# Kernel tuning notes

Measured on AMD Instinct MI355X. Metric: run time of the kernel, lower is better.

Reference implementation:

```python
import jax, jax.numpy as jnp
import numpy as np

B, T, F, H, L = 16384, 24, 7, 8, 4
DENSE = [T * H, 1024, 2048, 4]


def setup_inputs() -> dict:
    key = jax.random.key(0)
    d = {"x": jax.random.normal(jax.random.fold_in(key, 0), (B, T, F), jnp.float32)}
    k = 1
    s = 1.0 / np.sqrt(H)  # torch LSTM init bound
    for l in range(L):
        in_dim = F if l == 0 else H
        for name, shape in [("Wih", (4 * H, in_dim)), ("Whh", (4 * H, H)), ("bih", (4 * H,)), ("bhh", (4 * H,))]:
            d[f"{name}{l}"] = jax.random.uniform(jax.random.fold_in(key, k), shape, jnp.float32, -s, s)
            k += 1
    for i in range(1, len(DENSE)):
        si = 1.0 / np.sqrt(DENSE[i - 1])
        d[f"Wd{i}"] = jax.random.uniform(jax.random.fold_in(key, k), (DENSE[i], DENSE[i - 1]), jnp.float32, -si, si)
        k += 1
        d[f"bd{i}"] = jax.random.uniform(jax.random.fold_in(key, k), (DENSE[i],), jnp.float32, -si, si)
        k += 1
    return d


def _lstm_layer(xs, Wih, Whh, b):
    # xs: [T, B, in] -> ys: [T, B, H]; torch gate order i,f,g,o
    Hn = Whh.shape[1]
    h0 = jnp.zeros((xs.shape[1], Hn), xs.dtype)

    def step(carry, xt):
        h, c = carry
        z = xt @ Wih.T + h @ Whh.T + b  # [B, 4H]
        i, f, g, o = jnp.split(z, 4, axis=-1)
        c = jax.nn.sigmoid(f) * c + jax.nn.sigmoid(i) * jnp.tanh(g)
        h = jax.nn.sigmoid(o) * jnp.tanh(c)
        return (h, c), h

    (_, _), ys = jax.lax.scan(step, (h0, h0), xs)
    return ys


def _forward(x, lstm_params, dense_params):
    xs = jnp.transpose(x, (1, 0, 2))  # [T, B, F]
    for (Wih, Whh, bih, bhh) in lstm_params:
        xs = _lstm_layer(xs, Wih, Whh, bih + bhh)
    out = jnp.transpose(xs, (1, 0, 2)).reshape(x.shape[0], T * H)  # [B, 192]
    (W1, b1), (W2, b2), (W3, b3) = dense_params
    out = jax.nn.relu(out @ W1.T + b1)
    out = jax.nn.relu(out @ W2.T + b2)
    return out @ W3.T + b3  # [B, num_classes]


def reference(x, Wih0, Whh0, bih0, bhh0, Wih1, Whh1, bih1, bhh1, Wih2, Whh2, bih2, bhh2, Wih3, Whh3, bih3, bhh3, Wd1, bd1, Wd2, bd2, Wd3, bd3):
    lstm_params = [(Wih0, Whh0, bih0, bhh0), (Wih1, Whh1, bih1, bhh1), (Wih2, Whh2, bih2, bhh2), (Wih3, Whh3, bih3, bhh3)]
    dense_params = [(Wd1, bd1), (Wd2, bd2), (Wd3, bd3)]
    return _forward(x, lstm_params, dense_params)
```

## Files before the change

kernel.cpp:

```cpp
#include <hip/hip_runtime.h>
#include <hip/hip_bf16.h>

typedef __attribute__((ext_vector_type(4))) float f32x4;
typedef __attribute__((ext_vector_type(2))) float f32x2;
typedef __attribute__((ext_vector_type(8))) short bf16x8;

__device__ __forceinline__ ushort f2bf(float f) {
    union { float f; uint u; } v; v.f = f;
    uint u = v.u;
    return (ushort)((u + 0x7fffu + ((u >> 16) & 1u)) >> 16);
}
__device__ __forceinline__ float sigm(float x) {
    return __builtin_amdgcn_rcpf(1.0f + __builtin_amdgcn_exp2f(x * -1.442695040888963f));
}
__device__ __forceinline__ float tanh_(float x) {
    return 2.0f * __builtin_amdgcn_rcpf(1.0f + __builtin_amdgcn_exp2f(x * -2.885390081777927f)) - 1.0f;
}

typedef const __attribute__((address_space(1))) unsigned int ga_u32;
typedef __attribute__((address_space(3))) unsigned int lds_u32;
__device__ __forceinline__ void g2l16(const void* g, void* l) {
    __builtin_amdgcn_global_load_lds((ga_u32*)(unsigned long long)g,
                                     (lds_u32*)(unsigned int)(unsigned long long)l,
                                     16, 0, 0);
}

struct LstmW {
    const float* wih[4];
    const float* whh[4];
    const float* bih[4];
    const float* bhh[4];
};

__device__ __forceinline__ void gates8p(const f32x2 w01[8], const f32x2 w23[8],
                                        const float xv8[8], f32x2& a01, f32x2& a23) {
#pragma unroll
    for (int k = 0; k < 8; ++k) {
        f32x2 xv = {xv8[k], xv8[k]};
        a01 += w01[k] * xv;
        a23 += w23[k] * xv;
    }
}
__device__ __forceinline__ void cellup(f32x2 a01, f32x2 a23, float& h, float& c) {
    c = sigm(a01.y) * c + sigm(a01.x) * tanh_(a23.x);
    h = sigm(a23.y) * tanh_(c);
}
__device__ __forceinline__ void ld8(const float* p, float v[8]) {
    float4 a = *(const float4*)p;
    float4 b = *(const float4*)(p + 4);
    v[0] = a.x; v[1] = a.y; v[2] = a.z; v[3] = a.w;
    v[4] = b.x; v[5] = b.y; v[6] = b.z; v[7] = b.w;
}

__global__ __launch_bounds__(256) void pre_kernel(const float* __restrict__ x, LstmW p,
                                                  ushort* __restrict__ Y,
                                                  const float* __restrict__ W1,
                                                  const float* __restrict__ W2,
                                                  ushort* __restrict__ W1b,
                                                  ushort* __restrict__ W2b,
                                                  const float* __restrict__ b3,
                                                  float* __restrict__ out) {
    __shared__ float xs[32 * 168];
    __shared__ float hb[32 * 200];

    const int tid = threadIdx.x;
    if (blockIdx.x >= 512) {
        const int tg = (blockIdx.x - 512) * 256 + tid;
        if (tg < 16384) {
            float4 bv = {b3[0], b3[1], b3[2], b3[3]};
            ((float4*)out)[tg] = bv;
        }
#pragma unroll
        for (int s = 0; s < 4; ++s) {
            int i = tg + s * 143360;
            const float4* src; ushort4* dst; int off;
            if (i < 49152) { src = (const float4*)W1; dst = (ushort4*)W1b; off = i; }
            else { src = (const float4*)W2; dst = (ushort4*)W2b; off = i - 49152; }
            float4 v = src[off];
            ushort4 r; r.x = f2bf(v.x); r.y = f2bf(v.y); r.z = f2bf(v.z); r.w = f2bf(v.w);
            dst[off] = r;
        }
        return;
    }

    const int e0 = blockIdx.x * 32;
    {
        const float4* s = (const float4*)(x + (size_t)e0 * 168);
        float4* d = (float4*)xs;
        for (int i = tid; i < 1344; i += 256) d[i] = s[i];
    }
    __syncthreads();

    const int el = tid >> 3, j = tid & 7;
    float* hr = hb + el * 200;
    const float* xr = xs + el * 168;

    f32x2 wx01[8], wx23[8], wh01[8], wh23[8], b01, b23;

    {
        const float* Wih = p.wih[0];
        const float* Whh = p.whh[0];
#pragma unroll
        for (int k = 0; k < 7; ++k) {
            wx01[k] = {Wih[(0 + j) * 7 + k], Wih[(8 + j) * 7 + k]};
            wx23[k] = {Wih[(16 + j) * 7 + k], Wih[(24 + j) * 7 + k]};
        }
#pragma unroll
        for (int k = 0; k < 8; ++k) {
            wh01[k] = {Whh[(0 + j) * 8 + k], Whh[(8 + j) * 8 + k]};
            wh23[k] = {Whh[(16 + j) * 8 + k], Whh[(24 + j) * 8 + k]};
        }
        b01 = {p.bih[0][j] + p.bhh[0][j], p.bih[0][8 + j] + p.bhh[0][8 + j]};
        b23 = {p.bih[0][16 + j] + p.bhh[0][16 + j], p.bih[0][24 + j] + p.bhh[0][24 + j]};

        float h = 0.f, c = 0.f;
        {
            f32x2 a01 = b01, a23 = b23;
#pragma unroll
            for (int k = 0; k < 7; ++k) {
                f32x2 xv = {xr[k], xr[k]};
                a01 += wx01[k] * xv; a23 += wx23[k] * xv;
            }
            cellup(a01, a23, h, c);
            hr[j] = h;
        }
        for (int t = 1; t < 24; ++t) {
            f32x2 a01 = b01, a23 = b23;
#pragma unroll
            for (int k = 0; k < 7; ++k) {
                f32x2 xv = {xr[t * 7 + k], xr[t * 7 + k]};
                a01 += wx01[k] * xv; a23 += wx23[k] * xv;
            }
            float hp[8]; ld8(&hr[(t - 1) * 8], hp);
            gates8p(wh01, wh23, hp, a01, a23);
            cellup(a01, a23, h, c);
            hr[t * 8 + j] = h;
        }
    }

#pragma unroll
    for (int l = 1; l < 4; ++l) {
        const float* Wih = p.wih[l];
        const float* Whh = p.whh[l];
#pragma unroll
        for (int k = 0; k < 8; ++k) {
            wx01[k] = {Wih[(0 + j) * 8 + k], Wih[(8 + j) * 8 + k]};
            wx23[k] = {Wih[(16 + j) * 8 + k], Wih[(24 + j) * 8 + k]};
            wh01[k] = {Whh[(0 + j) * 8 + k], Whh[(8 + j) * 8 + k]};
            wh23[k] = {Whh[(16 + j) * 8 + k], Whh[(24 + j) * 8 + k]};
        }
        b01 = {p.bih[l][j] + p.bhh[l][j], p.bih[l][8 + j] + p.bhh[l][8 + j]};
        b23 = {p.bih[l][16 + j] + p.bhh[l][16 + j], p.bih[l][24 + j] + p.bhh[l][24 + j]};

        float h = 0.f, c = 0.f;
        {
            float xin[8]; ld8(&hr[0], xin);
            f32x2 a01 = b01, a23 = b23;
            gates8p(wx01, wx23, xin, a01, a23);
            cellup(a01, a23, h, c);
            hr[j] = h;
            if (l == 3) Y[((size_t)(e0 + el) * 24) * 8 + j] = f2bf(h);
        }
        for (int t = 1; t < 24; ++t) {
            float xin[8]; ld8(&hr[t * 8], xin);
            float hp[8];  ld8(&hr[(t - 1) * 8], hp);
            f32x2 a01 = b01, a23 = b23;
            gates8p(wx01, wx23, xin, a01, a23);
            gates8p(wh01, wh23, hp, a01, a23);
            cellup(a01, a23, h, c);
            hr[t * 8 + j] = h;
            if (l == 3) Y[((size_t)(e0 + el) * 24 + t) * 8 + j] = f2bf(h);
        }
    }
}

template <int KDIM, bool FUSE3>
__global__ __launch_bounds__(256) void gemm_kernel(const ushort* __restrict__ A,
                                                   const ushort* __restrict__ W,
                                                   const float* __restrict__ bias,
                                                   ushort* __restrict__ Hout,
                                                   const float* __restrict__ W3,
                                                   float* __restrict__ outf, int N) {
    constexpr int SMEMN = FUSE3 ? 17408 : 16384;
    __shared__ alignas(16) ushort smem[SMEMN];
    __shared__ alignas(16) float w3s[FUSE3 ? 528 : 1];
    ushort* As = smem;
    ushort* Ws = smem + 8192;

    const int tid = threadIdx.x;
    const int n0 = blockIdx.x * 128;
    const int m0 = blockIdx.y * 128;
    const int lane = tid & 63;
    const int wv = tid >> 6;
    const int wm = (wv & 1) * 64;
    const int wn = (wv >> 1) * 64;
    const int m16 = lane & 15;
    const int quad = lane >> 4;

    if (FUSE3) {
        for (int i = tid; i < 512; i += 256)
            w3s[(i >> 7) * 132 + (i & 127)] = W3[(size_t)(i >> 7) * 2048 + n0 + (i & 127)];
    }

    f32x4 acc[4][4];
    const f32x4 zero = {0.f, 0.f, 0.f, 0.f};
#pragma unroll
    for (int mi = 0; mi < 4; ++mi)
#pragma unroll
        for (int ni = 0; ni < 4; ++ni) acc[mi][ni] = zero;

    const int lrow = lane >> 3;
    const int lchunk = (lane & 7) ^ lrow;
    const ushort* Ag = A + (size_t)(m0 + wv * 32 + lrow) * KDIM + lchunk * 8;
    const ushort* Wg = W + (size_t)(n0 + wv * 32 + lrow) * KDIM + lchunk * 8;
    ushort* Ald = As + wv * 2048;
    ushort* Wld = Ws + wv * 2048;

    const int r7 = m16 & 7;
    const int ck0 = (quad ^ r7) * 8;
    const int ck1 = ((quad + 4) ^ r7) * 8;

    for (int k0 = 0; k0 < KDIM; k0 += 64) {
#pragma unroll
        for (int c = 0; c < 4; ++c)
            g2l16(Ag + (size_t)c * 8 * KDIM + k0, Ald + c * 512);
#pragma unroll
        for (int c = 0; c < 4; ++c)
            g2l16(Wg + (size_t)c * 8 * KDIM + k0, Wld + c * 512);
        __syncthreads();

#pragma unroll
        for (int kk = 0; kk < 2; ++kk) {
            const int ck = kk ? ck1 : ck0;
            bf16x8 bfr[4];
#pragma unroll
            for (int ni = 0; ni < 4; ++ni)
                bfr[ni] = *(const bf16x8*)&Ws[(wn + ni * 16 + m16) * 64 + ck];
#pragma unroll
            for (int mi = 0; mi < 4; ++mi) {
                bf16x8 afr = *(const bf16x8*)&As[(wm + mi * 16 + m16) * 64 + ck];
#pragma unroll
                for (int ni = 0; ni < 4; ++ni)
                    acc[mi][ni] = __builtin_amdgcn_mfma_f32_16x16x32_bf16(afr, bfr[ni],
                                                                         acc[mi][ni], 0, 0, 0);
            }
        }
        __syncthreads();
    }

    if (!FUSE3) {
#pragma unroll
        for (int ni = 0; ni < 4; ++ni) {
            const int col = n0 + wn + ni * 16 + m16;
            const float b = bias[col];
#pragma unroll
            for (int mi = 0; mi < 4; ++mi)
#pragma unroll
                for (int r = 0; r < 4; ++r) {
                    const int row = m0 + wm + mi * 16 + quad * 4 + r;
                    Hout[(size_t)row * N + col] = f2bf(fmaxf(acc[mi][ni][r] + b, 0.f));
                }
        }
    } else {
        float* Cs = (float*)smem;
        const int drow = tid >> 2;
        const int dn = tid & 3;
#pragma unroll
        for (int pass = 0; pass < 2; ++pass) {
            if ((wv & 1) == pass) {
#pragma unroll
                for (int ni = 0; ni < 4; ++ni) {
                    const int cl = wn + ni * 16 + m16;
                    const float b = bias[n0 + cl];
#pragma unroll
                    for (int mi = 0; mi < 4; ++mi)
#pragma unroll
                        for (int r = 0; r < 4; ++r) {
                            const int rl = mi * 16 + quad * 4 + r;
                            Cs[rl * 132 + cl] = fmaxf(acc[mi][ni][r] + b, 0.f);
                        }
                }
            }
            __syncthreads();
            const float* crow = &Cs[drow * 132];
            const float* wrow = &w3s[dn * 132];
            float p = 0.f;
#pragma unroll
            for (int ch = 0; ch < 32; ++ch) {
                f32x4 cv = *(const f32x4*)(crow + ch * 4);
                f32x4 wv4 = *(const f32x4*)(wrow + ch * 4);
                p += cv[0] * wv4[0] + cv[1] * wv4[1] + cv[2] * wv4[2] + cv[3] * wv4[3];
            }
            atomicAdd(&outf[(size_t)(m0 + pass * 64 + drow) * 4 + dn], p);
            __syncthreads();
        }
    }
}

extern "C" void kernel_launch(void* const* d_in, const int* in_sizes, int n_in,
                              void* d_out, int out_size, void* d_ws, size_t ws_size,
                              hipStream_t stream) {
    const float* x = (const float*)d_in[0];
    LstmW w;
    for (int l = 0; l < 4; ++l) {
        w.wih[l] = (const float*)d_in[1 + 4 * l];
        w.whh[l] = (const float*)d_in[2 + 4 * l];
        w.bih[l] = (const float*)d_in[3 + 4 * l];
        w.bhh[l] = (const float*)d_in[4 + 4 * l];
    }
    const float* Wd1 = (const float*)d_in[17];
    const float* bd1 = (const float*)d_in[18];
    const float* Wd2 = (const float*)d_in[19];
    const float* bd2 = (const float*)d_in[20];
    const float* Wd3 = (const float*)d_in[21];
    const float* bd3 = (const float*)d_in[22];
    float* out = (float*)d_out;

    ushort* Y   = (ushort*)d_ws;
    ushort* H1  = (ushort*)((char*)d_ws + 6291456);
    ushort* W1b = (ushort*)((char*)d_ws + 39845888);
    ushort* W2b = (ushort*)((char*)d_ws + 40239104);

    pre_kernel<<<1072, 256, 0, stream>>>(x, w, Y, Wd1, Wd2, W1b, W2b, bd3, out);
    gemm_kernel<192, false><<<dim3(8, 128), 256, 0, stream>>>(Y, W1b, bd1, H1, nullptr, nullptr, 1024);
    gemm_kernel<1024, true><<<dim3(16, 128), 256, 0, stream>>>(H1, W2b, bd2, nullptr, Wd3, out, 2048);
}
```

Before: 235.0 us.

## Load A fragments directly from global, stage only W in LDS, swap grid order

The GEMM kernels stop staging the activation tile A in shared memory. Each wave now reads its A fragments straight from global memory into registers, and only the weight tile goes through LDS. Shared memory use drops and launch bounds request 4 blocks per CU, to raise occupancy and remove LDS traffic for A. The grid is also transposed so consecutive blocks walk along M and share the same W tile in cache. The cost is more global/L2 traffic for A, since the two waves that share the same M rows each load it separately, and uncoalesced 16-byte row loads that may stall the MFMA pipeline.

```diff
diff --git a/kernel.cpp b/kernel.cpp
--- a/kernel.cpp
+++ b/kernel.cpp
@@ -175,21 +175,20 @@
 }
 
 template <int KDIM, bool FUSE3>
-__global__ __launch_bounds__(256) void gemm_kernel(const ushort* __restrict__ A,
-                                                   const ushort* __restrict__ W,
-                                                   const float* __restrict__ bias,
-                                                   ushort* __restrict__ Hout,
-                                                   const float* __restrict__ W3,
-                                                   float* __restrict__ outf, int N) {
-    constexpr int SMEMN = FUSE3 ? 17408 : 16384;
+__global__ __launch_bounds__(256, 4) void gemm_kernel(const ushort* __restrict__ A,
+                                                      const ushort* __restrict__ W,
+                                                      const float* __restrict__ bias,
+                                                      ushort* __restrict__ Hout,
+                                                      const float* __restrict__ W3,
+                                                      float* __restrict__ outf, int N) {
+    constexpr int SMEMN = FUSE3 ? 16896 : 8192;
     __shared__ alignas(16) ushort smem[SMEMN];
     __shared__ alignas(16) float w3s[FUSE3 ? 528 : 1];
-    ushort* As = smem;
-    ushort* Ws = smem + 8192;
+    ushort* Ws = smem;
 
     const int tid = threadIdx.x;
-    const int n0 = blockIdx.x * 128;
-    const int m0 = blockIdx.y * 128;
+    const int m0 = blockIdx.x * 128;
+    const int n0 = blockIdx.y * 128;
     const int lane = tid & 63;
     const int wv = tid >> 6;
     const int wm = (wv & 1) * 64;
@@ -202,49 +201,59 @@
             w3s[(i >> 7) * 132 + (i & 127)] = W3[(size_t)(i >> 7) * 2048 + n0 + (i & 127)];
     }
 
-    f32x4 acc[4][4];
-    const f32x4 zero = {0.f, 0.f, 0.f, 0.f};
-#pragma unroll
-    for (int mi = 0; mi < 4; ++mi)
-#pragma unroll
-        for (int ni = 0; ni < 4; ++ni) acc[mi][ni] = zero;
-
     const int lrow = lane >> 3;
     const int lchunk = (lane & 7) ^ lrow;
-    const ushort* Ag = A + (size_t)(m0 + wv * 32 + lrow) * KDIM + lchunk * 8;
     const ushort* Wg = W + (size_t)(n0 + wv * 32 + lrow) * KDIM + lchunk * 8;
-    ushort* Ald = As + wv * 2048;
     ushort* Wld = Ws + wv * 2048;
+
+    const ushort* Ar[4];
+#pragma unroll
+    for (int mi = 0; mi < 4; ++mi)
+        Ar[mi] = A + (size_t)(m0 + wm + mi * 16 + m16) * KDIM + quad * 8;
 
     const int r7 = m16 & 7;
     const int ck0 = (quad ^ r7) * 8;
     const int ck1 = ((quad + 4) ^ r7) * 8;
 
+    f32x4 acc[4][4];
+    const f32x4 zero = {0.f, 0.f, 0.f, 0.f};
+#pragma unroll
+    for (int mi = 0; mi < 4; ++mi)
+#pragma unroll
+        for (int ni = 0; ni < 4; ++ni) acc[mi][ni] = zero;
+
     for (int k0 = 0; k0 < KDIM; k0 += 64) {
-#pragma unroll
-        for (int c = 0; c < 4; ++c)
-            g2l16(Ag + (size_t)c * 8 * KDIM + k0, Ald + c * 512);
 #pragma unroll
         for (int c = 0; c < 4; ++c)
             g2l16(Wg + (size_t)c * 8 * KDIM + k0, Wld + c * 512);
+
+        bf16x8 afr0[4], afr1[4];
+#pragma unroll
+        for (int mi = 0; mi < 4; ++mi) {
+            afr0[mi] = *(const bf16x8*)(Ar[mi] + k0);
+            afr1[mi] = *(const bf16x8*)(Ar[mi] + k0 + 32);
+        }
         __syncthreads();
 
-#pragma unroll
-        for (int kk = 0; kk < 2; ++kk) {
-            const int ck = kk ? ck1 : ck0;
-            bf16x8 bfr[4];
+        bf16x8 bfr[4];
+#pragma unroll
+        for (int ni = 0; ni < 4; ++ni)
+            bfr[ni] = *(const bf16x8*)&Ws[(wn + ni * 16 + m16) * 64 + ck0];
+#pragma unroll
+        for (int mi = 0; mi < 4; ++mi)
 #pragma unroll
             for (int ni = 0; ni < 4; ++ni)
-                bfr[ni] = *(const bf16x8*)&Ws[(wn + ni * 16 + m16) * 64 + ck];
-#pragma unroll
-            for (int mi = 0; mi < 4; ++mi) {
-                bf16x8 afr = *(const bf16x8*)&As[(wm + mi * 16 + m16) * 64 + ck];
-#pragma unroll
-                for (int ni = 0; ni < 4; ++ni)
-                    acc[mi][ni] = __builtin_amdgcn_mfma_f32_16x16x32_bf16(afr, bfr[ni],
-                                                                         acc[mi][ni], 0, 0, 0);
-            }
-        }
+                acc[mi][ni] = __builtin_amdgcn_mfma_f32_16x16x32_bf16(afr0[mi], bfr[ni],
+                                                                     acc[mi][ni], 0, 0, 0);
+#pragma unroll
+        for (int ni = 0; ni < 4; ++ni)
+            bfr[ni] = *(const bf16x8*)&Ws[(wn + ni * 16 + m16) * 64 + ck1];
+#pragma unroll
+        for (int mi = 0; mi < 4; ++mi)
+#pragma unroll
+            for (int ni = 0; ni < 4; ++ni)
+                acc[mi][ni] = __builtin_amdgcn_mfma_f32_16x16x32_bf16(afr1[mi], bfr[ni],
+                                                                     acc[mi][ni], 0, 0, 0);
         __syncthreads();
     }
 
@@ -322,6 +331,6 @@
     ushort* W2b = (ushort*)((char*)d_ws + 40239104);
 
     pre_kernel<<<1072, 256, 0, stream>>>(x, w, Y, Wd1, Wd2, W1b, W2b, bd3, out);
-    gemm_kernel<192, false><<<dim3(8, 128), 256, 0, stream>>>(Y, W1b, bd1, H1, nullptr, nullptr, 1024);
-    gemm_kernel<1024, true><<<dim3(16, 128), 256, 0, stream>>>(H1, W2b, bd2, nullptr, Wd3, out, 2048);
-}
+    gemm_kernel<192, false><<<dim3(128, 8), 256, 0, stream>>>(Y, W1b, bd1, H1, nullptr, nullptr, 1024);
+    gemm_kernel<1024, true><<<dim3(128, 16), 256, 0, stream>>>(H1, W2b, bd2, nullptr, Wd3, out, 2048);
+}
```

Result: slower. 330.5 us (+40.7%).

## Switch dense GEMMs to 32x32x16 MFMA with swapped grid order

Applied to the files above, without the earlier changes.

Replaces the 16x16x32 bf16 MFMA tiling (4x4 accumulators per wave) with 32x32x16 MFMA (2x2 f32x16 accumulators), which reduces LDS fragment loads per MFMA. The grid is transposed so consecutive blocks share the same weight N-tile rather than the same A M-tile. Occupancy hints (launch_bounds 256,4) are added and the FUSE3 shared buffer is slightly shrunk. Epilogue row mapping is rewritten for the 32x32 output layout, which risks index errors and higher register pressure.

```diff
diff --git a/kernel.cpp b/kernel.cpp
--- a/kernel.cpp
+++ b/kernel.cpp
@@ -2,6 +2,7 @@
 #include <hip/hip_bf16.h>
 
 typedef __attribute__((ext_vector_type(4))) float f32x4;
+typedef __attribute__((ext_vector_type(16))) float f32x16;
 typedef __attribute__((ext_vector_type(2))) float f32x2;
 typedef __attribute__((ext_vector_type(8))) short bf16x8;
 
@@ -175,39 +176,32 @@
 }
 
 template <int KDIM, bool FUSE3>
-__global__ __launch_bounds__(256) void gemm_kernel(const ushort* __restrict__ A,
-                                                   const ushort* __restrict__ W,
-                                                   const float* __restrict__ bias,
-                                                   ushort* __restrict__ Hout,
-                                                   const float* __restrict__ W3,
-                                                   float* __restrict__ outf, int N) {
-    constexpr int SMEMN = FUSE3 ? 17408 : 16384;
+__device__ __forceinline__ void gemm_body(const ushort* __restrict__ A,
+                                          const ushort* __restrict__ W,
+                                          const float* __restrict__ bias,
+                                          ushort* __restrict__ Hout,
+                                          const float* __restrict__ W3,
+                                          float* __restrict__ outf, int N) {
+    constexpr int SMEMN = FUSE3 ? 16896 : 16384;
     __shared__ alignas(16) ushort smem[SMEMN];
     __shared__ alignas(16) float w3s[FUSE3 ? 528 : 1];
     ushort* As = smem;
     ushort* Ws = smem + 8192;
 
     const int tid = threadIdx.x;
-    const int n0 = blockIdx.x * 128;
-    const int m0 = blockIdx.y * 128;
+    const int m0 = blockIdx.x * 128;
+    const int n0 = blockIdx.y * 128;
     const int lane = tid & 63;
     const int wv = tid >> 6;
     const int wm = (wv & 1) * 64;
     const int wn = (wv >> 1) * 64;
-    const int m16 = lane & 15;
-    const int quad = lane >> 4;
+    const int l31 = lane & 31;
+    const int kh = lane >> 5;
 
     if (FUSE3) {
         for (int i = tid; i < 512; i += 256)
             w3s[(i >> 7) * 132 + (i & 127)] = W3[(size_t)(i >> 7) * 2048 + n0 + (i & 127)];
     }
-
-    f32x4 acc[4][4];
-    const f32x4 zero = {0.f, 0.f, 0.f, 0.f};
-#pragma unroll
-    for (int mi = 0; mi < 4; ++mi)
-#pragma unroll
-        for (int ni = 0; ni < 4; ++ni) acc[mi][ni] = zero;
 
     const int lrow = lane >> 3;
     const int lchunk = (lane & 7) ^ lrow;
@@ -216,9 +210,17 @@
     ushort* Ald = As + wv * 2048;
     ushort* Wld = Ws + wv * 2048;
 
-    const int r7 = m16 & 7;
-    const int ck0 = (quad ^ r7) * 8;
-    const int ck1 = ((quad + 4) ^ r7) * 8;
+    const int r7 = l31 & 7;
+    const int arow0 = (wm + l31) * 64;
+    const int brow0 = (wn + l31) * 64;
+
+    f32x16 acc[2][2];
+#pragma unroll
+    for (int mi = 0; mi < 2; ++mi)
+#pragma unroll
+        for (int ni = 0; ni < 2; ++ni)
+#pragma unroll
+            for (int r = 0; r < 16; ++r) acc[mi][ni][r] = 0.f;
 
     for (int k0 = 0; k0 < KDIM; k0 += 64) {
 #pragma unroll
@@ -230,34 +232,35 @@
         __syncthreads();
 
 #pragma unroll
-        for (int kk = 0; kk < 2; ++kk) {
-            const int ck = kk ? ck1 : ck0;
-            bf16x8 bfr[4];
-#pragma unroll
-            for (int ni = 0; ni < 4; ++ni)
-                bfr[ni] = *(const bf16x8*)&Ws[(wn + ni * 16 + m16) * 64 + ck];
-#pragma unroll
-            for (int mi = 0; mi < 4; ++mi) {
-                bf16x8 afr = *(const bf16x8*)&As[(wm + mi * 16 + m16) * 64 + ck];
-#pragma unroll
-                for (int ni = 0; ni < 4; ++ni)
-                    acc[mi][ni] = __builtin_amdgcn_mfma_f32_16x16x32_bf16(afr, bfr[ni],
+        for (int ks = 0; ks < 4; ++ks) {
+            const int ck = ((ks * 2 + kh) ^ r7) * 8;
+            bf16x8 afr[2], bfr[2];
+#pragma unroll
+            for (int mi = 0; mi < 2; ++mi)
+                afr[mi] = *(const bf16x8*)&As[arow0 + mi * 2048 + ck];
+#pragma unroll
+            for (int ni = 0; ni < 2; ++ni)
+                bfr[ni] = *(const bf16x8*)&Ws[brow0 + ni * 2048 + ck];
+#pragma unroll
+            for (int mi = 0; mi < 2; ++mi)
+#pragma unroll
+                for (int ni = 0; ni < 2; ++ni)
+                    acc[mi][ni] = __builtin_amdgcn_mfma_f32_32x32x16_bf16(afr[mi], bfr[ni],
                                                                          acc[mi][ni], 0, 0, 0);
-            }
         }
         __syncthreads();
     }
 
     if (!FUSE3) {
 #pragma unroll
-        for (int ni = 0; ni < 4; ++ni) {
-            const int col = n0 + wn + ni * 16 + m16;
+        for (int ni = 0; ni < 2; ++ni) {
+            const int col = n0 + wn + ni * 32 + l31;
             const float b = bias[col];
 #pragma unroll
-            for (int mi = 0; mi < 4; ++mi)
-#pragma unroll
-                for (int r = 0; r < 4; ++r) {
-                    const int row = m0 + wm + mi * 16 + quad * 4 + r;
+            for (int mi = 0; mi < 2; ++mi)
+#pragma unroll
+                for (int r = 0; r < 16; ++r) {
+                    const int row = m0 + wm + mi * 32 + (r & 3) + 8 * (r >> 2) + 4 * kh;
                     Hout[(size_t)row * N + col] = f2bf(fmaxf(acc[mi][ni][r] + b, 0.f));
                 }
         }
@@ -269,14 +272,14 @@
         for (int pass = 0; pass < 2; ++pass) {
             if ((wv & 1) == pass) {
 #pragma unroll
-                for (int ni = 0; ni < 4; ++ni) {
-                    const int cl = wn + ni * 16 + m16;
+                for (int ni = 0; ni < 2; ++ni) {
+                    const int cl = wn + ni * 32 + l31;
                     const float b = bias[n0 + cl];
 #pragma unroll
-                    for (int mi = 0; mi < 4; ++mi)
-#pragma unroll
-                        for (int r = 0; r < 4; ++r) {
-                            const int rl = mi * 16 + quad * 4 + r;
+                    for (int mi = 0; mi < 2; ++mi)
+#pragma unroll
+                        for (int r = 0; r < 16; ++r) {
+                            const int rl = mi * 32 + (r & 3) + 8 * (r >> 2) + 4 * kh;
                             Cs[rl * 132 + cl] = fmaxf(acc[mi][ni][r] + b, 0.f);
                         }
                 }
@@ -295,6 +298,20 @@
             __syncthreads();
         }
     }
+}
+
+__global__ __launch_bounds__(256, 4) void gemm1_kernel(const ushort* __restrict__ A,
+                                                       const ushort* __restrict__ W,
+                                                       const float* __restrict__ bias,
+                                                       ushort* __restrict__ Hout, int N) {
+    gemm_body<192, false>(A, W, bias, Hout, nullptr, nullptr, N);
+}
+__global__ __launch_bounds__(256, 4) void gemm2_kernel(const ushort* __restrict__ A,
+                                                       const ushort* __restrict__ W,
+                                                       const float* __restrict__ bias,
+                                                       const float* __restrict__ W3,
+                                                       float* __restrict__ outf) {
+    gemm_body<1024, true>(A, W, bias, nullptr, W3, outf, 2048);
 }
 
 extern "C" void kernel_launch(void* const* d_in, const int* in_sizes, int n_in,
@@ -322,6 +339,6 @@
     ushort* W2b = (ushort*)((char*)d_ws + 40239104);
 
     pre_kernel<<<1072, 256, 0, stream>>>(x, w, Y, Wd1, Wd2, W1b, W2b, bd3, out);
-    gemm_kernel<192, false><<<dim3(8, 128), 256, 0, stream>>>(Y, W1b, bd1, H1, nullptr, nullptr, 1024);
-    gemm_kernel<1024, true><<<dim3(16, 128), 256, 0, stream>>>(H1, W2b, bd2, nullptr, Wd3, out, 2048);
-}
+    gemm1_kernel<<<dim3(128, 8), 256, 0, stream>>>(Y, W1b, bd1, H1, 1024);
+    gemm2_kernel<<<dim3(128, 16), 256, 0, stream>>>(H1, W2b, bd2, Wd3, out);
+}
```

New measurement: 225.6 us (median of 2 runs). -4.0%, faster.
